# Optimization experiments

Hardware: AMD Instinct MI355X
Metric: run time of the kernel (lower is better)

Reference implementation:

```python
import jax, jax.numpy as jnp
import numpy as np

N = 524288            # total ray samples
EMB_DIM = 32          # hash embedder out_dim (16 levels x 2 feats)
DIR_DIM = 27          # freq embedder out_dim (3 + 3*2*4)
GEO_FEAT = 15         # cfg.geo_feature_dim
LATENT_DIM = 128      # cfg.latent_code_dim
NUM_LATENT = 100      # cfg.num_latent_code
D_HIDDEN = 64
RGB_IN = EMB_DIM + DIR_DIM + GEO_FEAT + LATENT_DIM  # 202


def setup_inputs() -> dict:
    key = jax.random.key(0)
    ks = jax.random.split(key, 16)

    def lin(k, fan_in, fan_out):
        # torch nn.Linear default init: U(-1/sqrt(fan_in), 1/sqrt(fan_in))
        bound = 1.0 / np.sqrt(fan_in)
        kw, kb = jax.random.split(k)
        W = jax.random.uniform(kw, (fan_in, fan_out), jnp.float32, -bound, bound)
        b = jax.random.uniform(kb, (fan_out,), jnp.float32, -bound, bound)
        return W, b

    occ_W0, occ_b0 = lin(ks[0], EMB_DIM, D_HIDDEN)
    occ_W1, occ_b1 = lin(ks[1], D_HIDDEN, D_HIDDEN)
    occ_W2, occ_b2 = lin(ks[2], D_HIDDEN, 1 + GEO_FEAT)
    rgb_W0, rgb_b0 = lin(ks[3], RGB_IN, D_HIDDEN)
    rgb_W1, rgb_b1 = lin(ks[4], D_HIDDEN, D_HIDDEN)
    rgb_W2, rgb_b2 = lin(ks[5], D_HIDDEN, 3)

    # kaiming_normal_ init of rgb_latent
    rgb_latent = jax.random.normal(ks[6], (NUM_LATENT, LATENT_DIM), jnp.float32) * np.sqrt(2.0 / LATENT_DIM)

    embedded = jax.random.normal(ks[7], (N, EMB_DIM), jnp.float32)
    embedded_dir = jax.random.normal(ks[8], (N, DIR_DIM), jnp.float32)

    return {
        'embedded': embedded, 'embedded_dir': embedded_dir,
        'occ_W0': occ_W0, 'occ_b0': occ_b0,
        'occ_W1': occ_W1, 'occ_b1': occ_b1,
        'occ_W2': occ_W2, 'occ_b2': occ_b2,
        'rgb_W0': rgb_W0, 'rgb_b0': rgb_b0,
        'rgb_W1': rgb_W1, 'rgb_b1': rgb_b1,
        'rgb_W2': rgb_W2, 'rgb_b2': rgb_b2,
        'rgb_latent': rgb_latent,
        'latent_index': 7,
    }


def reference(embedded, embedded_dir,
              occ_W0, occ_b0, occ_W1, occ_b1, occ_W2, occ_b2,
              rgb_W0, rgb_b0, rgb_W1, rgb_b1, rgb_W2, rgb_b2,
              rgb_latent, latent_index):
    sp = jax.nn.softplus
    # occ MLP: softplus hidden layers, linear output
    h = sp(embedded @ occ_W0 + occ_b0)
    h = sp(h @ occ_W1 + occ_b1)
    hidden = h @ occ_W2 + occ_b2                     # [N, 1+GEO_FEAT]
    occ = 1.0 - jnp.exp(-sp(hidden[:, :1]))          # [N, 1]
    feature = hidden[:, 1:]                          # [N, GEO_FEAT]
    # latent gather: one latent code broadcast over all N samples
    n = embedded.shape[0]
    latent = jnp.broadcast_to(rgb_latent[latent_index], (n, rgb_latent.shape[1]))
    x = jnp.concatenate([embedded, embedded_dir, feature, latent], axis=-1)  # [N, 202]
    # rgb MLP
    r = sp(x @ rgb_W0 + rgb_b0)
    r = sp(r @ rgb_W1 + rgb_b1)
    rgb = jax.nn.sigmoid(r @ rgb_W2 + rgb_b2)        # [N, 3]
    raw = jnp.concatenate([rgb, occ], axis=-1)       # [N, 4]
    return raw, occ
```

## Files before the change

kernel.cpp:

```cpp
#include <hip/hip_runtime.h>

typedef __bf16 bf16x8 __attribute__((ext_vector_type(8)));
typedef float f32x4 __attribute__((ext_vector_type(4)));
typedef unsigned int u32x4 __attribute__((ext_vector_type(4)));
typedef unsigned int u32x2 __attribute__((ext_vector_type(2)));
typedef u32x4 u32x4a __attribute__((may_alias));
typedef u32x2 u32x2a __attribute__((may_alias));
typedef f32x4 f32x4a __attribute__((may_alias));
typedef unsigned int u32a __attribute__((may_alias));

#define NITER 4

__device__ inline unsigned short f2b(float f) {
    unsigned int x;
    __builtin_memcpy(&x, &f, 4);
    unsigned int r = (x + 0x7FFFu + ((x >> 16) & 1u)) >> 16;
    return (unsigned short)r;
}
__device__ inline unsigned int cvt_pk_bf16(float lo, float hi) {
    unsigned int r;
    asm("v_cvt_pk_bf16_f32 %0, %1, %2" : "=v"(r) : "v"(lo), "v"(hi));
    return r;
}
__device__ inline float vexp2(float x) { float r; asm("v_exp_f32 %0, %1" : "=v"(r) : "v"(x)); return r; }
__device__ inline float vlog2(float x) { float r; asm("v_log_f32 %0, %1" : "=v"(r) : "v"(x)); return r; }
__device__ inline float vrcp(float x)  { float r; asm("v_rcp_f32 %0, %1" : "=v"(r) : "v"(x)); return r; }
__device__ inline float softplus_f(float x) {
    return 0.69314718f * vlog2(1.f + vexp2(1.44269504f * x));
}
__device__ inline float sigmoid_f(float x) {
    return vrcp(1.f + vexp2(-1.44269504f * x));
}
__device__ inline bf16x8 as_bf16x8(u32x4 v) { return __builtin_bit_cast(bf16x8, v); }

#define SPST(dstp, acc) { \
    u32x2 pk_ = {cvt_pk_bf16(softplus_f((acc)[0]), softplus_f((acc)[1])), \
                 cvt_pk_bf16(softplus_f((acc)[2]), softplus_f((acc)[3]))}; \
    *(u32x2a*)(dstp) = pk_; }


__global__ __launch_bounds__(256) void prep_weights(
    const float* __restrict__ oW0, const float* __restrict__ ob0,
    const float* __restrict__ oW1, const float* __restrict__ ob1,
    const float* __restrict__ oW2, const float* __restrict__ ob2,
    const float* __restrict__ rW0, const float* __restrict__ rb0,
    const float* __restrict__ rW1, const float* __restrict__ rb1,
    const float* __restrict__ rW2, const float* __restrict__ rb2,
    const float* __restrict__ rlat, const int* __restrict__ lidx,
    float* __restrict__ wsf, ushort* __restrict__ wsw)
{
    const int bid = blockIdx.x, tid = threadIdx.x;
    __shared__ float red[256];

    if (bid == 0) {
        for (int i = tid; i < 224; i += 256) {
            float v;
            if (i < 64)       v = ob0[i];
            else if (i < 128) v = ob1[i - 64];
            else if (i < 144) v = ob2[i - 128];
            else if (i < 208) v = rb1[i - 144];
            else              v = (i - 208 < 3) ? rb2[i - 208] : 0.f;
            wsf[i] = v;
        }
    }
    if (bid == 7) {
        const int outn = tid & 63, sl = tid >> 6;
        const float* lat = rlat + (size_t)lidx[0] * 128;
        float p = 0.f;
        for (int k = sl * 32; k < sl * 32 + 32; k++)
            p = fmaf(lat[k], rW0[(74 + k) * 64 + outn], p);
        red[tid] = p;
        __syncthreads();
        if (tid < 64)
            wsf[224 + tid] = rb0[tid] + red[tid] + red[64 + tid] + red[128 + tid] + red[192 + tid];
    }
    for (int t = tid; t < 288; t += 256) {
        const int s = bid * 288 + t;
        const int frag = s >> 6, lane = s & 63;
        const int qq = lane >> 4, cc = lane & 15;
        const float* W;
        int ldn = 64, nt = 0, kt = 0;
        bool isr0 = false, isr2 = false;
        if (frag < 4)       { W = oW0; nt = frag; kt = 0; }
        else if (frag < 12) { W = oW1; int f = frag - 4;  nt = f >> 1; kt = f & 1; }
        else if (frag < 14) { W = oW2; ldn = 16; nt = 0; kt = frag - 12; }
        else if (frag < 26) { W = rW0; int f = frag - 14; nt = f / 3; kt = f - nt * 3; isr0 = true; }
        else if (frag < 34) { W = rW1; int f = frag - 26; nt = f >> 1; kt = f & 1; }
        else                { W = rW2; ldn = 3; nt = 0; kt = frag - 34; isr2 = true; }
        const int nn = nt * 16 + cc;
        __align__(16) ushort vals[8];
#pragma unroll
        for (int j = 0; j < 8; j++) {
            int k = kt * 32 + qq * 8 + j;
            float v = 0.f;
            if (isr0) {
                int ks = -1;
                if (k < 59) ks = k;
                else if (k >= 65 && k < 80) ks = k - 65 + 59;
                if (ks >= 0) v = W[ks * 64 + nn];
            } else if (isr2) {
                if (nn < 3) v = W[k * 3 + nn];
            } else {
                v = W[k * ldn + nn];
            }
            vals[j] = f2b(v);
        }
        *(u32x4a*)&wsw[s * 8] = *(const u32x4a*)vals;
    }
}

__global__ __launch_bounds__(512, 4) void net_mfma(
    const float* __restrict__ emb, const float* __restrict__ dir,
    const float* __restrict__ wsf, const ushort* __restrict__ wsw,
    float* __restrict__ out, int n)
{
    __shared__ __align__(16) ushort s_w[36 * 64 * 8];
    __shared__ __align__(16) ushort s_h[8][32 * 72];
    __shared__ __align__(16) float s_b[288];

    const int tid = threadIdx.x;
    for (int i = tid; i < 36 * 64; i += 512)
        *(u32x4a*)&s_w[i * 8] = *(const u32x4a*)(wsw + i * 8);
    for (int i = tid; i < 288; i += 512) s_b[i] = wsf[i];
    __syncthreads();

    const int wave = tid >> 6, lane = tid & 63, q = lane >> 4, c = lane & 15;
    ushort* hw = s_h[wave];
    ushort* hA = hw + c * 72;
    ushort* hB = hw + (c + 16) * 72;
    for (int i = lane; i < 1152; i += 64) ((u32a*)hw)[i] = 0u;

    const int q4 = q * 4, q8 = q * 8;
    const long dlim = (long)n * 27;

    for (int it = 0; it < NITER; ++it) {
        const ushort* sw = s_w;
        const float*  sb = s_b;
        asm volatile("" : "+v"(sw), "+v"(sb));

        const long p0 = (long)blockIdx.x * 1024 + it * 256 + wave * 32;

        bf16x8 x_embA, x_embB, x_dirA, x_dirB;
        {
            const float* ep = emb + (p0 + c) * 32 + q8;
            f32x4 e0 = *(const f32x4a*)ep;
            f32x4 e1 = *(const f32x4a*)(ep + 4);
            u32x4 pk = {cvt_pk_bf16(e0[0], e0[1]), cvt_pk_bf16(e0[2], e0[3]),
                        cvt_pk_bf16(e1[0], e1[1]), cvt_pk_bf16(e1[2], e1[3])};
            x_embA = as_bf16x8(pk);
            const float* ep2 = emb + (p0 + 16 + c) * 32 + q8;
            f32x4 f0 = *(const f32x4a*)ep2;
            f32x4 f1 = *(const f32x4a*)(ep2 + 4);
            u32x4 pk2 = {cvt_pk_bf16(f0[0], f0[1]), cvt_pk_bf16(f0[2], f0[3]),
                         cvt_pk_bf16(f1[0], f1[1]), cvt_pk_bf16(f1[2], f1[3])};
            x_embB = as_bf16x8(pk2);
        }
        {
            const long ibA = (p0 + c) * 27 + q8;
            f32x4 d0, d1;
            if (ibA + 8 <= dlim) {
                d0 = *(const f32x4a*)(dir + ibA);
                d1 = *(const f32x4a*)(dir + ibA + 4);
            } else {
#pragma unroll
                for (int j = 0; j < 4; j++) d0[j] = (ibA + j < dlim) ? dir[ibA + j] : 0.f;
#pragma unroll
                for (int j = 0; j < 4; j++) d1[j] = (ibA + 4 + j < dlim) ? dir[ibA + 4 + j] : 0.f;
            }
            u32x4 pk = {cvt_pk_bf16(d0[0], d0[1]), cvt_pk_bf16(d0[2], d0[3]),
                        cvt_pk_bf16(d1[0], d1[1]), cvt_pk_bf16(d1[2], d1[3])};
            x_dirA = as_bf16x8(pk);
            const long ibB = (p0 + 16 + c) * 27 + q8;
            f32x4 g0, g1;
            if (ibB + 8 <= dlim) {
                g0 = *(const f32x4a*)(dir + ibB);
                g1 = *(const f32x4a*)(dir + ibB + 4);
            } else {
#pragma unroll
                for (int j = 0; j < 4; j++) g0[j] = (ibB + j < dlim) ? dir[ibB + j] : 0.f;
#pragma unroll
                for (int j = 0; j < 4; j++) g1[j] = (ibB + 4 + j < dlim) ? dir[ibB + 4 + j] : 0.f;
            }
            u32x4 pk2 = {cvt_pk_bf16(g0[0], g0[1]), cvt_pk_bf16(g0[2], g0[3]),
                         cvt_pk_bf16(g1[0], g1[1]), cvt_pk_bf16(g1[2], g1[3])};
            x_dirB = as_bf16x8(pk2);
        }

#pragma unroll
        for (int nt = 0; nt < 4; ++nt) {
            bf16x8 w = as_bf16x8(*(const u32x4a*)&sw[((0 + nt) * 64 + lane) * 8]);
            f32x4 b = *(const f32x4a*)&sb[0 + nt * 16 + q4];
            f32x4 aA = __builtin_amdgcn_mfma_f32_16x16x32_bf16(w, x_embA, b, 0, 0, 0);
            f32x4 aB = __builtin_amdgcn_mfma_f32_16x16x32_bf16(w, x_embB, b, 0, 0, 0);
            SPST(&hA[nt * 16 + q4], aA);
            SPST(&hB[nt * 16 + q4], aB);
        }
        {
            bf16x8 hA0 = as_bf16x8(*(const u32x4a*)&hA[0 + q8]);
            bf16x8 hA1 = as_bf16x8(*(const u32x4a*)&hA[32 + q8]);
            bf16x8 hB0 = as_bf16x8(*(const u32x4a*)&hB[0 + q8]);
            bf16x8 hB1 = as_bf16x8(*(const u32x4a*)&hB[32 + q8]);
#pragma unroll
            for (int nt = 0; nt < 4; ++nt) {
                bf16x8 w0 = as_bf16x8(*(const u32x4a*)&sw[((4 + nt * 2 + 0) * 64 + lane) * 8]);
                bf16x8 w1 = as_bf16x8(*(const u32x4a*)&sw[((4 + nt * 2 + 1) * 64 + lane) * 8]);
                f32x4 b = *(const f32x4a*)&sb[64 + nt * 16 + q4];
                f32x4 aA = __builtin_amdgcn_mfma_f32_16x16x32_bf16(w0, hA0, b, 0, 0, 0);
                aA = __builtin_amdgcn_mfma_f32_16x16x32_bf16(w1, hA1, aA, 0, 0, 0);
                f32x4 aB = __builtin_amdgcn_mfma_f32_16x16x32_bf16(w0, hB0, b, 0, 0, 0);
                aB = __builtin_amdgcn_mfma_f32_16x16x32_bf16(w1, hB1, aB, 0, 0, 0);
                SPST(&hA[nt * 16 + q4], aA);
                SPST(&hB[nt * 16 + q4], aB);
            }
        }
        float occA, occB;
        {
            bf16x8 hA0 = as_bf16x8(*(const u32x4a*)&hA[0 + q8]);
            bf16x8 hA1 = as_bf16x8(*(const u32x4a*)&hA[32 + q8]);
            bf16x8 hB0 = as_bf16x8(*(const u32x4a*)&hB[0 + q8]);
            bf16x8 hB1 = as_bf16x8(*(const u32x4a*)&hB[32 + q8]);
            bf16x8 w0 = as_bf16x8(*(const u32x4a*)&sw[(12 * 64 + lane) * 8]);
            bf16x8 w1 = as_bf16x8(*(const u32x4a*)&sw[(13 * 64 + lane) * 8]);
            f32x4 b = *(const f32x4a*)&sb[128 + q4];
            f32x4 aA = __builtin_amdgcn_mfma_f32_16x16x32_bf16(w0, hA0, b, 0, 0, 0);
            aA = __builtin_amdgcn_mfma_f32_16x16x32_bf16(w1, hA1, aA, 0, 0, 0);
            f32x4 aB = __builtin_amdgcn_mfma_f32_16x16x32_bf16(w0, hB0, b, 0, 0, 0);
            aB = __builtin_amdgcn_mfma_f32_16x16x32_bf16(w1, hB1, aB, 0, 0, 0);
            occA = sigmoid_f(aA[0]);
            occB = sigmoid_f(aB[0]);
            u32x2 pkA = {cvt_pk_bf16(aA[0], aA[1]), cvt_pk_bf16(aA[2], aA[3])};
            *(u32x2a*)&hA[q4] = pkA;
            u32x2 pkB = {cvt_pk_bf16(aB[0], aB[1]), cvt_pk_bf16(aB[2], aB[3])};
            *(u32x2a*)&hB[q4] = pkB;
        }
        {
            bf16x8 xfA = as_bf16x8(*(const u32x4a*)&hA[q8]);
            bf16x8 xfB = as_bf16x8(*(const u32x4a*)&hB[q8]);
#pragma unroll
            for (int nt = 0; nt < 4; ++nt) {
                bf16x8 w0 = as_bf16x8(*(const u32x4a*)&sw[((14 + nt * 3 + 0) * 64 + lane) * 8]);
                bf16x8 w1 = as_bf16x8(*(const u32x4a*)&sw[((14 + nt * 3 + 1) * 64 + lane) * 8]);
                bf16x8 w2 = as_bf16x8(*(const u32x4a*)&sw[((14 + nt * 3 + 2) * 64 + lane) * 8]);
                f32x4 b = *(const f32x4a*)&sb[224 + nt * 16 + q4];
                f32x4 aA = __builtin_amdgcn_mfma_f32_16x16x32_bf16(w0, x_embA, b, 0, 0, 0);
                aA = __builtin_amdgcn_mfma_f32_16x16x32_bf16(w1, x_dirA, aA, 0, 0, 0);
                aA = __builtin_amdgcn_mfma_f32_16x16x32_bf16(w2, xfA, aA, 0, 0, 0);
                f32x4 aB = __builtin_amdgcn_mfma_f32_16x16x32_bf16(w0, x_embB, b, 0, 0, 0);
                aB = __builtin_amdgcn_mfma_f32_16x16x32_bf16(w1, x_dirB, aB, 0, 0, 0);
                aB = __builtin_amdgcn_mfma_f32_16x16x32_bf16(w2, xfB, aB, 0, 0, 0);
                SPST(&hA[nt * 16 + q4], aA);
                SPST(&hB[nt * 16 + q4], aB);
            }
        }
        {
            bf16x8 hA0 = as_bf16x8(*(const u32x4a*)&hA[0 + q8]);
            bf16x8 hA1 = as_bf16x8(*(const u32x4a*)&hA[32 + q8]);
            bf16x8 hB0 = as_bf16x8(*(const u32x4a*)&hB[0 + q8]);
            bf16x8 hB1 = as_bf16x8(*(const u32x4a*)&hB[32 + q8]);
#pragma unroll
            for (int nt = 0; nt < 4; ++nt) {
                bf16x8 w0 = as_bf16x8(*(const u32x4a*)&sw[((26 + nt * 2 + 0) * 64 + lane) * 8]);
                bf16x8 w1 = as_bf16x8(*(const u32x4a*)&sw[((26 + nt * 2 + 1) * 64 + lane) * 8]);
                f32x4 b = *(const f32x4a*)&sb[144 + nt * 16 + q4];
                f32x4 aA = __builtin_amdgcn_mfma_f32_16x16x32_bf16(w0, hA0, b, 0, 0, 0);
                aA = __builtin_amdgcn_mfma_f32_16x16x32_bf16(w1, hA1, aA, 0, 0, 0);
                f32x4 aB = __builtin_amdgcn_mfma_f32_16x16x32_bf16(w0, hB0, b, 0, 0, 0);
                aB = __builtin_amdgcn_mfma_f32_16x16x32_bf16(w1, hB1, aB, 0, 0, 0);
                SPST(&hA[nt * 16 + q4], aA);
                SPST(&hB[nt * 16 + q4], aB);
            }
        }
        {
            bf16x8 hA0 = as_bf16x8(*(const u32x4a*)&hA[0 + q8]);
            bf16x8 hA1 = as_bf16x8(*(const u32x4a*)&hA[32 + q8]);
            bf16x8 hB0 = as_bf16x8(*(const u32x4a*)&hB[0 + q8]);
            bf16x8 hB1 = as_bf16x8(*(const u32x4a*)&hB[32 + q8]);
            bf16x8 w0 = as_bf16x8(*(const u32x4a*)&sw[(34 * 64 + lane) * 8]);
            bf16x8 w1 = as_bf16x8(*(const u32x4a*)&sw[(35 * 64 + lane) * 8]);
            f32x4 b = *(const f32x4a*)&sb[208 + q4];
            f32x4 aA = __builtin_amdgcn_mfma_f32_16x16x32_bf16(w0, hA0, b, 0, 0, 0);
            aA = __builtin_amdgcn_mfma_f32_16x16x32_bf16(w1, hA1, aA, 0, 0, 0);
            f32x4 aB = __builtin_amdgcn_mfma_f32_16x16x32_bf16(w0, hB0, b, 0, 0, 0);
            aB = __builtin_amdgcn_mfma_f32_16x16x32_bf16(w1, hB1, aB, 0, 0, 0);
            if (q == 0) {
                f32x4 oA;
                oA[0] = sigmoid_f(aA[0]);
                oA[1] = sigmoid_f(aA[1]);
                oA[2] = sigmoid_f(aA[2]);
                oA[3] = occA;
                *(f32x4a*)&out[(p0 + c) * 4] = oA;
                out[(long)4 * n + p0 + c] = occA;
                f32x4 oB;
                oB[0] = sigmoid_f(aB[0]);
                oB[1] = sigmoid_f(aB[1]);
                oB[2] = sigmoid_f(aB[2]);
                oB[3] = occB;
                *(f32x4a*)&out[(p0 + 16 + c) * 4] = oB;
                out[(long)4 * n + p0 + 16 + c] = occB;
            }
        }
    }
}

extern "C" void kernel_launch(void* const* d_in, const int* in_sizes, int n_in,
                              void* d_out, int out_size, void* d_ws, size_t ws_size,
                              hipStream_t stream) {
    const int n = in_sizes[0] / 32;
    float*  wsf = (float*)d_ws;
    ushort* wsw = (ushort*)((char*)d_ws + 1152);
    prep_weights<<<8, 256, 0, stream>>>(
        (const float*)d_in[2], (const float*)d_in[3],
        (const float*)d_in[4], (const float*)d_in[5],
        (const float*)d_in[6], (const float*)d_in[7],
        (const float*)d_in[8], (const float*)d_in[9],
        (const float*)d_in[10], (const float*)d_in[11],
        (const float*)d_in[12], (const float*)d_in[13],
        (const float*)d_in[14], (const int*)d_in[15],
        wsf, wsw);
    net_mfma<<<n / 1024, 512, 0, stream>>>(
        (const float*)d_in[0], (const float*)d_in[1],
        wsf, wsw, (float*)d_out, n);
}
```

Baseline: 207.6 us.

## Pass MLP activations between layers via ds_bpermute instead of LDS scratch

Drops the per-wave shared-memory activation buffer. MFMA output fragments are now reshuffled into the next layer's input layout with ds_bpermute cross-lane gathers, held in registers. The freed LDS lets the launch bound rise to 7 blocks per CU, and each block does 2 iterations instead of 4, doubling the grid. The trade-off is extra permute instructions, more register pressure under the tighter occupancy bound, and more blocks each reloading the weights into LDS.

```diff
diff --git a/kernel.cpp b/kernel.cpp
--- a/kernel.cpp
+++ b/kernel.cpp
@@ -9,7 +9,7 @@
 typedef f32x4 f32x4a __attribute__((may_alias));
 typedef unsigned int u32a __attribute__((may_alias));
 
-#define NITER 4
+#define NITER 2
 
 __device__ inline unsigned short f2b(float f) {
     unsigned int x;
@@ -33,10 +33,32 @@
 }
 __device__ inline bf16x8 as_bf16x8(u32x4 v) { return __builtin_bit_cast(bf16x8, v); }
 
-#define SPST(dstp, acc) { \
-    u32x2 pk_ = {cvt_pk_bf16(softplus_f((acc)[0]), softplus_f((acc)[1])), \
-                 cvt_pk_bf16(softplus_f((acc)[2]), softplus_f((acc)[3]))}; \
-    *(u32x2a*)(dstp) = pk_; }
+__device__ inline u32x2 sp_pk(f32x4 acc) {
+    u32x2 r = {cvt_pk_bf16(softplus_f(acc[0]), softplus_f(acc[1])),
+               cvt_pk_bf16(softplus_f(acc[2]), softplus_f(acc[3]))};
+    return r;
+}
+
+__device__ inline u32x4 gather8(u32x2 lo, u32x2 hi, int idx0, int idx1, bool hisel) {
+    int a0 = __builtin_amdgcn_ds_bpermute(idx0, (int)lo[0]);
+    int b0 = __builtin_amdgcn_ds_bpermute(idx0, (int)hi[0]);
+    int a1 = __builtin_amdgcn_ds_bpermute(idx0, (int)lo[1]);
+    int b1 = __builtin_amdgcn_ds_bpermute(idx0, (int)hi[1]);
+    int a2 = __builtin_amdgcn_ds_bpermute(idx1, (int)lo[0]);
+    int b2 = __builtin_amdgcn_ds_bpermute(idx1, (int)hi[0]);
+    int a3 = __builtin_amdgcn_ds_bpermute(idx1, (int)lo[1]);
+    int b3 = __builtin_amdgcn_ds_bpermute(idx1, (int)hi[1]);
+    u32x4 r = {(unsigned)(hisel ? b0 : a0), (unsigned)(hisel ? b1 : a1),
+               (unsigned)(hisel ? b2 : a2), (unsigned)(hisel ? b3 : a3)};
+    return r;
+}
+__device__ inline u32x4 gather4(u32x2 a, int idx0, int idx1) {
+    u32x4 r = {(unsigned)__builtin_amdgcn_ds_bpermute(idx0, (int)a[0]),
+               (unsigned)__builtin_amdgcn_ds_bpermute(idx0, (int)a[1]),
+               (unsigned)__builtin_amdgcn_ds_bpermute(idx1, (int)a[0]),
+               (unsigned)__builtin_amdgcn_ds_bpermute(idx1, (int)a[1])};
+    return r;
+}
 
 
 __global__ __launch_bounds__(256) void prep_weights(
@@ -109,13 +131,12 @@
     }
 }
 
-__global__ __launch_bounds__(512, 4) void net_mfma(
+__global__ __launch_bounds__(512, 7) void net_mfma(
     const float* __restrict__ emb, const float* __restrict__ dir,
     const float* __restrict__ wsf, const ushort* __restrict__ wsw,
     float* __restrict__ out, int n)
 {
     __shared__ __align__(16) ushort s_w[36 * 64 * 8];
-    __shared__ __align__(16) ushort s_h[8][32 * 72];
     __shared__ __align__(16) float s_b[288];
 
     const int tid = threadIdx.x;
@@ -125,12 +146,10 @@
     __syncthreads();
 
     const int wave = tid >> 6, lane = tid & 63, q = lane >> 4, c = lane & 15;
-    ushort* hw = s_h[wave];
-    ushort* hA = hw + c * 72;
-    ushort* hB = hw + (c + 16) * 72;
-    for (int i = lane; i < 1152; i += 64) ((u32a*)hw)[i] = 0u;
-
     const int q4 = q * 4, q8 = q * 8;
+    const bool hisel = q >= 2;
+    const int idx0 = ((((lane >> 4) & 1) << 5) | c) << 2;
+    const int idx1 = idx0 | 64;
     const long dlim = (long)n * 27;
 
     for (int it = 0; it < NITER; ++it) {
@@ -138,7 +157,7 @@
         const float*  sb = s_b;
         asm volatile("" : "+v"(sw), "+v"(sb));
 
-        const long p0 = (long)blockIdx.x * 1024 + it * 256 + wave * 32;
+        const long p0 = (long)blockIdx.x * 512 + it * 256 + wave * 32;
 
         bf16x8 x_embA, x_embB, x_dirA, x_dirB;
         {
@@ -186,102 +205,101 @@
             x_dirB = as_bf16x8(pk2);
         }
 
+        u32x2 pkA[4], pkB[4];
+
 #pragma unroll
         for (int nt = 0; nt < 4; ++nt) {
             bf16x8 w = as_bf16x8(*(const u32x4a*)&sw[((0 + nt) * 64 + lane) * 8]);
             f32x4 b = *(const f32x4a*)&sb[0 + nt * 16 + q4];
             f32x4 aA = __builtin_amdgcn_mfma_f32_16x16x32_bf16(w, x_embA, b, 0, 0, 0);
             f32x4 aB = __builtin_amdgcn_mfma_f32_16x16x32_bf16(w, x_embB, b, 0, 0, 0);
-            SPST(&hA[nt * 16 + q4], aA);
-            SPST(&hB[nt * 16 + q4], aB);
-        }
-        {
-            bf16x8 hA0 = as_bf16x8(*(const u32x4a*)&hA[0 + q8]);
-            bf16x8 hA1 = as_bf16x8(*(const u32x4a*)&hA[32 + q8]);
-            bf16x8 hB0 = as_bf16x8(*(const u32x4a*)&hB[0 + q8]);
-            bf16x8 hB1 = as_bf16x8(*(const u32x4a*)&hB[32 + q8]);
-#pragma unroll
-            for (int nt = 0; nt < 4; ++nt) {
-                bf16x8 w0 = as_bf16x8(*(const u32x4a*)&sw[((4 + nt * 2 + 0) * 64 + lane) * 8]);
-                bf16x8 w1 = as_bf16x8(*(const u32x4a*)&sw[((4 + nt * 2 + 1) * 64 + lane) * 8]);
-                f32x4 b = *(const f32x4a*)&sb[64 + nt * 16 + q4];
-                f32x4 aA = __builtin_amdgcn_mfma_f32_16x16x32_bf16(w0, hA0, b, 0, 0, 0);
-                aA = __builtin_amdgcn_mfma_f32_16x16x32_bf16(w1, hA1, aA, 0, 0, 0);
-                f32x4 aB = __builtin_amdgcn_mfma_f32_16x16x32_bf16(w0, hB0, b, 0, 0, 0);
-                aB = __builtin_amdgcn_mfma_f32_16x16x32_bf16(w1, hB1, aB, 0, 0, 0);
-                SPST(&hA[nt * 16 + q4], aA);
-                SPST(&hB[nt * 16 + q4], aB);
-            }
-        }
-        float occA, occB;
-        {
-            bf16x8 hA0 = as_bf16x8(*(const u32x4a*)&hA[0 + q8]);
-            bf16x8 hA1 = as_bf16x8(*(const u32x4a*)&hA[32 + q8]);
-            bf16x8 hB0 = as_bf16x8(*(const u32x4a*)&hB[0 + q8]);
-            bf16x8 hB1 = as_bf16x8(*(const u32x4a*)&hB[32 + q8]);
-            bf16x8 w0 = as_bf16x8(*(const u32x4a*)&sw[(12 * 64 + lane) * 8]);
-            bf16x8 w1 = as_bf16x8(*(const u32x4a*)&sw[(13 * 64 + lane) * 8]);
-            f32x4 b = *(const f32x4a*)&sb[128 + q4];
+            pkA[nt] = sp_pk(aA);
+            pkB[nt] = sp_pk(aB);
+        }
+        bf16x8 hA0 = as_bf16x8(gather8(pkA[0], pkA[1], idx0, idx1, hisel));
+        bf16x8 hA1 = as_bf16x8(gather8(pkA[2], pkA[3], idx0, idx1, hisel));
+        bf16x8 hB0 = as_bf16x8(gather8(pkB[0], pkB[1], idx0, idx1, hisel));
+        bf16x8 hB1 = as_bf16x8(gather8(pkB[2], pkB[3], idx0, idx1, hisel));
+
+#pragma unroll
+        for (int nt = 0; nt < 4; ++nt) {
+            bf16x8 w0 = as_bf16x8(*(const u32x4a*)&sw[((4 + nt * 2 + 0) * 64 + lane) * 8]);
+            bf16x8 w1 = as_bf16x8(*(const u32x4a*)&sw[((4 + nt * 2 + 1) * 64 + lane) * 8]);
+            f32x4 b = *(const f32x4a*)&sb[64 + nt * 16 + q4];
             f32x4 aA = __builtin_amdgcn_mfma_f32_16x16x32_bf16(w0, hA0, b, 0, 0, 0);
             aA = __builtin_amdgcn_mfma_f32_16x16x32_bf16(w1, hA1, aA, 0, 0, 0);
             f32x4 aB = __builtin_amdgcn_mfma_f32_16x16x32_bf16(w0, hB0, b, 0, 0, 0);
             aB = __builtin_amdgcn_mfma_f32_16x16x32_bf16(w1, hB1, aB, 0, 0, 0);
+            pkA[nt] = sp_pk(aA);
+            pkB[nt] = sp_pk(aB);
+        }
+        bf16x8 gA0 = as_bf16x8(gather8(pkA[0], pkA[1], idx0, idx1, hisel));
+        bf16x8 gA1 = as_bf16x8(gather8(pkA[2], pkA[3], idx0, idx1, hisel));
+        bf16x8 gB0 = as_bf16x8(gather8(pkB[0], pkB[1], idx0, idx1, hisel));
+        bf16x8 gB1 = as_bf16x8(gather8(pkB[2], pkB[3], idx0, idx1, hisel));
+
+        float occA, occB;
+        bf16x8 xfA, xfB;
+        {
+            bf16x8 w0 = as_bf16x8(*(const u32x4a*)&sw[(12 * 64 + lane) * 8]);
+            bf16x8 w1 = as_bf16x8(*(const u32x4a*)&sw[(13 * 64 + lane) * 8]);
+            f32x4 b = *(const f32x4a*)&sb[128 + q4];
+            f32x4 aA = __builtin_amdgcn_mfma_f32_16x16x32_bf16(w0, gA0, b, 0, 0, 0);
+            aA = __builtin_amdgcn_mfma_f32_16x16x32_bf16(w1, gA1, aA, 0, 0, 0);
+            f32x4 aB = __builtin_amdgcn_mfma_f32_16x16x32_bf16(w0, gB0, b, 0, 0, 0);
+            aB = __builtin_amdgcn_mfma_f32_16x16x32_bf16(w1, gB1, aB, 0, 0, 0);
             occA = sigmoid_f(aA[0]);
             occB = sigmoid_f(aB[0]);
-            u32x2 pkA = {cvt_pk_bf16(aA[0], aA[1]), cvt_pk_bf16(aA[2], aA[3])};
-            *(u32x2a*)&hA[q4] = pkA;
-            u32x2 pkB = {cvt_pk_bf16(aB[0], aB[1]), cvt_pk_bf16(aB[2], aB[3])};
-            *(u32x2a*)&hB[q4] = pkB;
-        }
+            u32x2 p2A = {cvt_pk_bf16(aA[0], aA[1]), cvt_pk_bf16(aA[2], aA[3])};
+            u32x2 p2B = {cvt_pk_bf16(aB[0], aB[1]), cvt_pk_bf16(aB[2], aB[3])};
+            xfA = as_bf16x8(gather4(p2A, idx0, idx1));
+            xfB = as_bf16x8(gather4(p2B, idx0, idx1));
+        }
+#pragma unroll
+        for (int nt = 0; nt < 4; ++nt) {
+            bf16x8 w0 = as_bf16x8(*(const u32x4a*)&sw[((14 + nt * 3 + 0) * 64 + lane) * 8]);
+            bf16x8 w1 = as_bf16x8(*(const u32x4a*)&sw[((14 + nt * 3 + 1) * 64 + lane) * 8]);
+            bf16x8 w2 = as_bf16x8(*(const u32x4a*)&sw[((14 + nt * 3 + 2) * 64 + lane) * 8]);
+            f32x4 b = *(const f32x4a*)&sb[224 + nt * 16 + q4];
+            f32x4 aA = __builtin_amdgcn_mfma_f32_16x16x32_bf16(w0, x_embA, b, 0, 0, 0);
+            aA = __builtin_amdgcn_mfma_f32_16x16x32_bf16(w1, x_dirA, aA, 0, 0, 0);
+            aA = __builtin_amdgcn_mfma_f32_16x16x32_bf16(w2, xfA, aA, 0, 0, 0);
+            f32x4 aB = __builtin_amdgcn_mfma_f32_16x16x32_bf16(w0, x_embB, b, 0, 0, 0);
+            aB = __builtin_amdgcn_mfma_f32_16x16x32_bf16(w1, x_dirB, aB, 0, 0, 0);
+            aB = __builtin_amdgcn_mfma_f32_16x16x32_bf16(w2, xfB, aB, 0, 0, 0);
+            pkA[nt] = sp_pk(aA);
+            pkB[nt] = sp_pk(aB);
+        }
+        bf16x8 rA0 = as_bf16x8(gather8(pkA[0], pkA[1], idx0, idx1, hisel));
+        bf16x8 rA1 = as_bf16x8(gather8(pkA[2], pkA[3], idx0, idx1, hisel));
+        bf16x8 rB0 = as_bf16x8(gather8(pkB[0], pkB[1], idx0, idx1, hisel));
+        bf16x8 rB1 = as_bf16x8(gather8(pkB[2], pkB[3], idx0, idx1, hisel));
+
+#pragma unroll
+        for (int nt = 0; nt < 4; ++nt) {
+            bf16x8 w0 = as_bf16x8(*(const u32x4a*)&sw[((26 + nt * 2 + 0) * 64 + lane) * 8]);
+            bf16x8 w1 = as_bf16x8(*(const u32x4a*)&sw[((26 + nt * 2 + 1) * 64 + lane) * 8]);
+            f32x4 b = *(const f32x4a*)&sb[144 + nt * 16 + q4];
+            f32x4 aA = __builtin_amdgcn_mfma_f32_16x16x32_bf16(w0, rA0, b, 0, 0, 0);
+            aA = __builtin_amdgcn_mfma_f32_16x16x32_bf16(w1, rA1, aA, 0, 0, 0);
+            f32x4 aB = __builtin_amdgcn_mfma_f32_16x16x32_bf16(w0, rB0, b, 0, 0, 0);
+            aB = __builtin_amdgcn_mfma_f32_16x16x32_bf16(w1, rB1, aB, 0, 0, 0);
+            pkA[nt] = sp_pk(aA);
+            pkB[nt] = sp_pk(aB);
+        }
+        bf16x8 sA0 = as_bf16x8(gather8(pkA[0], pkA[1], idx0, idx1, hisel));
+        bf16x8 sA1 = as_bf16x8(gather8(pkA[2], pkA[3], idx0, idx1, hisel));
+        bf16x8 sB0 = as_bf16x8(gather8(pkB[0], pkB[1], idx0, idx1, hisel));
+        bf16x8 sB1 = as_bf16x8(gather8(pkB[2], pkB[3], idx0, idx1, hisel));
+
         {
-            bf16x8 xfA = as_bf16x8(*(const u32x4a*)&hA[q8]);
-            bf16x8 xfB = as_bf16x8(*(const u32x4a*)&hB[q8]);
-#pragma unroll
-            for (int nt = 0; nt < 4; ++nt) {
-                bf16x8 w0 = as_bf16x8(*(const u32x4a*)&sw[((14 + nt * 3 + 0) * 64 + lane) * 8]);
-                bf16x8 w1 = as_bf16x8(*(const u32x4a*)&sw[((14 + nt * 3 + 1) * 64 + lane) * 8]);
-                bf16x8 w2 = as_bf16x8(*(const u32x4a*)&sw[((14 + nt * 3 + 2) * 64 + lane) * 8]);
-                f32x4 b = *(const f32x4a*)&sb[224 + nt * 16 + q4];
-                f32x4 aA = __builtin_amdgcn_mfma_f32_16x16x32_bf16(w0, x_embA, b, 0, 0, 0);
-                aA = __builtin_amdgcn_mfma_f32_16x16x32_bf16(w1, x_dirA, aA, 0, 0, 0);
-                aA = __builtin_amdgcn_mfma_f32_16x16x32_bf16(w2, xfA, aA, 0, 0, 0);
-                f32x4 aB = __builtin_amdgcn_mfma_f32_16x16x32_bf16(w0, x_embB, b, 0, 0, 0);
-                aB = __builtin_amdgcn_mfma_f32_16x16x32_bf16(w1, x_dirB, aB, 0, 0, 0);
-                aB = __builtin_amdgcn_mfma_f32_16x16x32_bf16(w2, xfB, aB, 0, 0, 0);
-                SPST(&hA[nt * 16 + q4], aA);
-                SPST(&hB[nt * 16 + q4], aB);
-            }
-        }
-        {
-            bf16x8 hA0 = as_bf16x8(*(const u32x4a*)&hA[0 + q8]);
-            bf16x8 hA1 = as_bf16x8(*(const u32x4a*)&hA[32 + q8]);
-            bf16x8 hB0 = as_bf16x8(*(const u32x4a*)&hB[0 + q8]);
-            bf16x8 hB1 = as_bf16x8(*(const u32x4a*)&hB[32 + q8]);
-#pragma unroll
-            for (int nt = 0; nt < 4; ++nt) {
-                bf16x8 w0 = as_bf16x8(*(const u32x4a*)&sw[((26 + nt * 2 + 0) * 64 + lane) * 8]);
-                bf16x8 w1 = as_bf16x8(*(const u32x4a*)&sw[((26 + nt * 2 + 1) * 64 + lane) * 8]);
-                f32x4 b = *(const f32x4a*)&sb[144 + nt * 16 + q4];
-                f32x4 aA = __builtin_amdgcn_mfma_f32_16x16x32_bf16(w0, hA0, b, 0, 0, 0);
-                aA = __builtin_amdgcn_mfma_f32_16x16x32_bf16(w1, hA1, aA, 0, 0, 0);
-                f32x4 aB = __builtin_amdgcn_mfma_f32_16x16x32_bf16(w0, hB0, b, 0, 0, 0);
-                aB = __builtin_amdgcn_mfma_f32_16x16x32_bf16(w1, hB1, aB, 0, 0, 0);
-                SPST(&hA[nt * 16 + q4], aA);
-                SPST(&hB[nt * 16 + q4], aB);
-            }
-        }
-        {
-            bf16x8 hA0 = as_bf16x8(*(const u32x4a*)&hA[0 + q8]);
-            bf16x8 hA1 = as_bf16x8(*(const u32x4a*)&hA[32 + q8]);
-            bf16x8 hB0 = as_bf16x8(*(const u32x4a*)&hB[0 + q8]);
-            bf16x8 hB1 = as_bf16x8(*(const u32x4a*)&hB[32 + q8]);
             bf16x8 w0 = as_bf16x8(*(const u32x4a*)&sw[(34 * 64 + lane) * 8]);
             bf16x8 w1 = as_bf16x8(*(const u32x4a*)&sw[(35 * 64 + lane) * 8]);
             f32x4 b = *(const f32x4a*)&sb[208 + q4];
-            f32x4 aA = __builtin_amdgcn_mfma_f32_16x16x32_bf16(w0, hA0, b, 0, 0, 0);
-            aA = __builtin_amdgcn_mfma_f32_16x16x32_bf16(w1, hA1, aA, 0, 0, 0);
-            f32x4 aB = __builtin_amdgcn_mfma_f32_16x16x32_bf16(w0, hB0, b, 0, 0, 0);
-            aB = __builtin_amdgcn_mfma_f32_16x16x32_bf16(w1, hB1, aB, 0, 0, 0);
+            f32x4 aA = __builtin_amdgcn_mfma_f32_16x16x32_bf16(w0, sA0, b, 0, 0, 0);
+            aA = __builtin_amdgcn_mfma_f32_16x16x32_bf16(w1, sA1, aA, 0, 0, 0);
+            f32x4 aB = __builtin_amdgcn_mfma_f32_16x16x32_bf16(w0, sB0, b, 0, 0, 0);
+            aB = __builtin_amdgcn_mfma_f32_16x16x32_bf16(w1, sB1, aB, 0, 0, 0);
             if (q == 0) {
                 f32x4 oA;
                 oA[0] = sigmoid_f(aA[0]);
@@ -317,7 +335,7 @@
         (const float*)d_in[12], (const float*)d_in[13],
         (const float*)d_in[14], (const int*)d_in[15],
         wsf, wsw);
-    net_mfma<<<n / 1024, 512, 0, stream>>>(
+    net_mfma<<<n / 512, 512, 0, stream>>>(
         (const float*)d_in[0], (const float*)d_in[1],
         wsf, wsw, (float*)d_out, n);
 }
```

New measurement: 239.1 us. +15.2%, slower.
